# Optimization experiments

Hardware: AMD Instinct MI355X
Metric: run time of the kernel (lower is better)

Reference implementation:

```python
import jax, jax.numpy as jnp
import numpy as np

B, D_TCF, T, GAF_DIM, DK, HIDDEN, N_CLASSES = 128, 512, 1024, 256, 32, 64, 4
EPS = 1e-5

def _glorot(key, shape):
    fan_out, fan_in = shape
    lim = float(np.sqrt(6.0 / (fan_in + fan_out)))
    return jax.random.uniform(key, shape, jnp.float32, -lim, lim)

def setup_inputs() -> dict:
    key = jax.random.key(0)
    ks = jax.random.split(key, 8)
    return {
        "tcf_feat": jax.random.normal(ks[0], (B, D_TCF, T), jnp.float32),
        "gaf_emb": jax.random.normal(ks[1], (B, GAF_DIM), jnp.float32),
        "Wq": _glorot(ks[2], (DK, D_TCF)),        # q_proj.weight [out,in]
        "Wkv": _glorot(ks[3], (DK, GAF_DIM)),     # kv_proj.weight
        "Wout": _glorot(ks[4], (D_TCF, DK)),      # out_proj.weight
        "ln1_g": jnp.ones((D_TCF,), jnp.float32),
        "ln1_b": jnp.zeros((D_TCF,), jnp.float32),
        "W1": _glorot(ks[5], (HIDDEN, D_TCF)),
        "b1": jnp.zeros((HIDDEN,), jnp.float32),
        "ln2_g": jnp.ones((HIDDEN,), jnp.float32),
        "ln2_b": jnp.zeros((HIDDEN,), jnp.float32),
        "W2": _glorot(ks[6], (N_CLASSES, HIDDEN)),
        "b2": jnp.zeros((N_CLASSES,), jnp.float32),
    }

def _layernorm(x, g, b):
    mu = jnp.mean(x, axis=-1, keepdims=True)
    var = jnp.mean(jnp.square(x - mu), axis=-1, keepdims=True)
    return (x - mu) * jax.lax.rsqrt(var + EPS) * g + b

def reference(tcf_feat, gaf_emb, Wq, Wkv, Wout, ln1_g, ln1_b, W1, b1, ln2_g, ln2_b, W2, b2):
    scale = DK ** (-0.5)
    x = jnp.swapaxes(tcf_feat, 1, 2)                      # [B,T,d_tcf]
    Q = jnp.einsum('btd,kd->btk', x, Wq)                  # [B,T,dk]
    KV = gaf_emb @ Wkv.T                                  # [B,dk] (single key/value)
    scores = jnp.einsum('btk,bk->bt', Q, KV) * scale      # [B,T]
    w = jax.nn.softmax(scores, axis=1)                    # softmax over T (dim=1)
    attn_out = w[:, :, None] * KV[:, None, :]             # [B,T,dk]
    y = _layernorm(x + jnp.einsum('btk,dk->btd', attn_out, Wout), ln1_g, ln1_b)
    pooled = jnp.mean(y, axis=1)                          # [B,d_tcf]
    h = jax.nn.elu(_layernorm(pooled @ W1.T + b1, ln2_g, ln2_b))
    return h @ W2.T + b2                                  # [B,n_classes]
```

## Files before the change

kernel.cpp:

```cpp
#include <hip/hip_runtime.h>

#define BN 128
#define DTCF 512
#define TT 1024
#define GAF 256
#define DKK 32
#define HID 64
#define NCLS 4
#define LNEPS 1e-5f
#define SCALE 0.17677669529663687f

typedef float f4v __attribute__((ext_vector_type(4)));

__global__ __launch_bounds__(1024, 4) void k_fusedA(
    const float* __restrict__ tcf, const float* __restrict__ gaf,
    const float* __restrict__ Wq, const float* __restrict__ Wkv,
    const float* __restrict__ Wout, const float* __restrict__ W1,
    float* __restrict__ u, float* __restrict__ muu,
    float* __restrict__ r_o, float* __restrict__ S2, float* __restrict__ S3,
    float* __restrict__ W1t)
{
    int b = blockIdx.x, tid = threadIdx.x;

    if (b >= BN) {
        int e0 = (b - BN) * 4096 + tid * 4;
        int j  = e0 >> 9;
        int dd = e0 & 511;
        #pragma unroll
        for (int i = 0; i < 4; ++i)
            W1t[(dd + i) * HID + j] = W1[j * DTCF + dd + i];
        return;
    }

    __shared__ float gaf_s[GAF];
    __shared__ float kvp[DKK][8];
    __shared__ float kv_s[DKK];
    __shared__ float2 uq_s[DTCF];
    __shared__ float red[32];
    __shared__ float stats[2];

    int lane = tid & 63, wv = tid >> 6;

    if (tid < GAF) gaf_s[tid] = gaf[b * GAF + tid];
    __syncthreads();

    if ((tid & 31) < 8) {
        int k = tid >> 5, p8 = tid & 7;
        float a = 0.f;
        #pragma unroll
        for (int g = p8 * 32; g < p8 * 32 + 32; ++g)
            a += gaf_s[g] * Wkv[k * GAF + g];
        kvp[k][p8] = a;
    }
    __syncthreads();
    if (tid < DKK) {
        float a = 0.f;
        #pragma unroll
        for (int p = 0; p < 8; ++p) a += kvp[tid][p];
        kv_s[tid] = a;
    }
    __syncthreads();

    if (tid < DTCF) {
        int d = tid;
        float uu = 0.f;
        #pragma unroll
        for (int k = 0; k < DKK; ++k) uu += kv_s[k] * Wout[d * DKK + k];
        uq_s[d].x = uu;
        u[b * DTCF + d] = uu;
        float su = uu, suu = uu * uu;
        #pragma unroll
        for (int off = 32; off > 0; off >>= 1) {
            su  += __shfl_down(su, off);
            suu += __shfl_down(suu, off);
        }
        if (lane == 0) { red[wv] = su; red[16 + wv] = suu; }
    } else {
        int d = tid - DTCF;
        float qq = 0.f;
        #pragma unroll
        for (int k = 0; k < DKK; ++k) qq += kv_s[k] * Wq[k * DTCF + d];
        uq_s[d].y = qq;
    }
    __syncthreads();
    if (tid == 0) {
        float s = 0.f, ss = 0.f;
        #pragma unroll
        for (int i = 0; i < 8; ++i) { s += red[i]; ss += red[16 + i]; }
        float m = s * (1.f / DTCF);
        stats[0] = m;
        stats[1] = ss * (1.f / DTCF) - m * m;
        muu[b] = m;
    }
    __syncthreads();
    float mu_u = stats[0], var_u = stats[1];

    const float* col = tcf + (size_t)b * (DTCF * TT) + tid;
    float sx = 0.f, sxx = 0.f, sxu = 0.f, sxq = 0.f;
    #pragma unroll 16
    for (int d = 0; d < DTCF; ++d) {
        float v = col[d << 10];
        float2 uq = uq_s[d];
        sx  += v;
        sxx += v * v;
        sxu += v * uq.x;
        sxq += v * uq.y;
    }

    const float inv_d = 1.f / DTCF;
    float mx = sx * inv_d;
    float vx = sxx * inv_d - mx * mx;
    float cv = sxu * inv_d - mx * mu_u;
    float sc = sxq * SCALE;

    float m = sc;
    #pragma unroll
    for (int off = 32; off > 0; off >>= 1) m = fmaxf(m, __shfl_xor(m, off));
    if (lane == 0) red[wv] = m;
    __syncthreads();
    m = red[0];
    #pragma unroll
    for (int i = 1; i < 16; ++i) m = fmaxf(m, red[i]);

    float e = __expf(sc - m);
    float s = e;
    #pragma unroll
    for (int off = 32; off > 0; off >>= 1) s += __shfl_xor(s, off);
    if (lane == 0) red[16 + wv] = s;
    __syncthreads();
    s = 0.f;
    #pragma unroll
    for (int i = 0; i < 16; ++i) s += red[16 + i];
    float inv = 1.f / s;

    float w  = e * inv;
    float vr = vx + 2.f * w * cv + w * w * var_u;
    float rr = rsqrtf(vr + LNEPS);
    r_o[b * TT + tid] = rr;

    float s2p = rr * w, s3p = rr * mx;
    #pragma unroll
    for (int off = 32; off > 0; off >>= 1) {
        s2p += __shfl_xor(s2p, off);
        s3p += __shfl_xor(s3p, off);
    }
    __syncthreads();
    if (lane == 0) { red[wv] = s2p; red[16 + wv] = s3p; }
    __syncthreads();
    if (tid == 0) {
        float a2 = 0.f, a3 = 0.f;
        #pragma unroll
        for (int i = 0; i < 16; ++i) { a2 += red[i]; a3 += red[16 + i]; }
        S2[b] = a2 * (1.f / TT);
        S3[b] = a3 * (1.f / TT);
    }
}

__global__ __launch_bounds__(256) void k_passB(
    const float* __restrict__ tcf, const float* __restrict__ r,
    const float* __restrict__ u, const float* __restrict__ muu,
    const float* __restrict__ S2, const float* __restrict__ S3,
    const float* __restrict__ g1, const float* __restrict__ be1,
    float* __restrict__ pooled)
{
    int b = blockIdx.x, yb = blockIdx.y;
    int tid = threadIdx.x, wv = tid >> 6, lane = tid & 63;
    int d = (DTCF - 4) - yb * 4 + wv;

    const float* row = tcf + ((size_t)b * DTCF + d) * TT;
    const float* rb  = r + (size_t)b * TT;

    float acc = 0.f;
    #pragma unroll
    for (int i = 0; i < 4; ++i) {
        f4v    x  = __builtin_nontemporal_load((const f4v*)(row + i * 256 + lane * 4));
        float4 rv = *(const float4*)(rb + i * 256 + lane * 4);
        acc += rv.x * x.x + rv.y * x.y + rv.z * x.z + rv.w * x.w;
    }
    for (int off = 32; off > 0; off >>= 1) acc += __shfl_down(acc, off);

    if (lane == 0) {
        float pd = acc * (1.f / TT) - S3[b] + (u[b * DTCF + d] - muu[b]) * S2[b];
        pooled[b * DTCF + d] = g1[d] * pd + be1[d];
    }
}

__global__ __launch_bounds__(256) void k_head(
    const float* __restrict__ pooled, const float* __restrict__ W1t,
    const float* __restrict__ b1, const float* __restrict__ g2,
    const float* __restrict__ be2, const float* __restrict__ W2,
    const float* __restrict__ b2o, float* __restrict__ out)
{
    int b = blockIdx.x, tid = threadIdx.x;
    int j = tid & 63, wv = tid >> 6;
    __shared__ float p_s[DTCF];
    __shared__ float hred[4][HID];
    for (int i = tid; i < DTCF; i += 256) p_s[i] = pooled[b * DTCF + i];
    __syncthreads();

    float hp = 0.f;
    #pragma unroll 8
    for (int i = 0; i < 128; ++i) {
        int dd = wv * 128 + i;
        hp += p_s[dd] * W1t[dd * HID + j];
    }
    hred[wv][j] = hp;
    __syncthreads();

    if (wv == 0) {
        float h = hred[0][j] + hred[1][j] + hred[2][j] + hred[3][j] + b1[j];
        float mu = h;
        for (int off = 32; off > 0; off >>= 1) mu += __shfl_xor(mu, off);
        mu *= (1.f / HID);
        float df = h - mu;
        float vr = df * df;
        for (int off = 32; off > 0; off >>= 1) vr += __shfl_xor(vr, off);
        vr *= (1.f / HID);
        float hn = df * rsqrtf(vr + LNEPS) * g2[j] + be2[j];
        float he = hn > 0.f ? hn : expm1f(hn);

        #pragma unroll
        for (int c = 0; c < NCLS; ++c) {
            float v = he * W2[c * HID + j];
            for (int off = 32; off > 0; off >>= 1) v += __shfl_xor(v, off);
            if (j == 0) out[b * NCLS + c] = v + b2o[c];
        }
    }
}

extern "C" void kernel_launch(void* const* d_in, const int* in_sizes, int n_in,
                              void* d_out, int out_size, void* d_ws, size_t ws_size,
                              hipStream_t stream)
{
    const float* tcf  = (const float*)d_in[0];
    const float* gaf  = (const float*)d_in[1];
    const float* Wq   = (const float*)d_in[2];
    const float* Wkv  = (const float*)d_in[3];
    const float* Wout = (const float*)d_in[4];
    const float* ln1g = (const float*)d_in[5];
    const float* ln1b = (const float*)d_in[6];
    const float* W1   = (const float*)d_in[7];
    const float* b1   = (const float*)d_in[8];
    const float* ln2g = (const float*)d_in[9];
    const float* ln2b = (const float*)d_in[10];
    const float* W2   = (const float*)d_in[11];
    const float* b2   = (const float*)d_in[12];

    float* ws     = (float*)d_ws;
    float* u      = ws;
    float* muu    = u + BN * DTCF;
    float* r      = muu + BN;
    float* S2     = r + BN * TT;
    float* S3     = S2 + BN;
    float* pooled = S3 + BN;
    float* W1t    = pooled + BN * DTCF;

    k_fusedA<<<BN + 8, 1024, 0, stream>>>(tcf, gaf, Wq, Wkv, Wout, W1,
                                          u, muu, r, S2, S3, W1t);
    k_passB<<<dim3(BN, DTCF / 4), 256, 0, stream>>>(tcf, r, u, muu, S2, S3,
                                                    ln1g, ln1b, pooled);
    k_head<<<BN, 256, 0, stream>>>(pooled, W1t, b1, ln2g, ln2b, W2, b2,
                                   (float*)d_out);
}
```

Baseline: 424.4 us.

## Split pass-A statistics over two D halves and add separate softmax kernel

The column-statistics pass is split across two blocks per batch, each covering half of the feature dimension, which doubles the grid from 128 to 256 blocks of 1024 threads. Partial sums go to a workspace buffer and a new small kernel combines them, computes the u statistics, softmax, LayerNorm reciprocals and the S2/S3 reductions, and transposes W1. The aim is better CU occupancy on a 256-CU-class GPU, at the cost of an extra launch and an extra round trip of partial sums through global memory.

```diff
diff --git a/kernel.cpp b/kernel.cpp
--- a/kernel.cpp
+++ b/kernel.cpp
@@ -12,40 +12,24 @@
 
 typedef float f4v __attribute__((ext_vector_type(4)));
 
-__global__ __launch_bounds__(1024, 4) void k_fusedA(
+__global__ __launch_bounds__(1024) void k_A(
     const float* __restrict__ tcf, const float* __restrict__ gaf,
     const float* __restrict__ Wq, const float* __restrict__ Wkv,
-    const float* __restrict__ Wout, const float* __restrict__ W1,
-    float* __restrict__ u, float* __restrict__ muu,
-    float* __restrict__ r_o, float* __restrict__ S2, float* __restrict__ S3,
-    float* __restrict__ W1t)
-{
-    int b = blockIdx.x, tid = threadIdx.x;
-
-    if (b >= BN) {
-        int e0 = (b - BN) * 4096 + tid * 4;
-        int j  = e0 >> 9;
-        int dd = e0 & 511;
-        #pragma unroll
-        for (int i = 0; i < 4; ++i)
-            W1t[(dd + i) * HID + j] = W1[j * DTCF + dd + i];
-        return;
-    }
+    const float* __restrict__ Wout,
+    float* __restrict__ u, float* __restrict__ part)
+{
+    int b = blockIdx.x, h = blockIdx.y, tid = threadIdx.x;
 
     __shared__ float gaf_s[GAF];
     __shared__ float kvp[DKK][8];
     __shared__ float kv_s[DKK];
-    __shared__ float2 uq_s[DTCF];
-    __shared__ float red[32];
-    __shared__ float stats[2];
-
-    int lane = tid & 63, wv = tid >> 6;
+    __shared__ float2 uq_s[256];
 
     if (tid < GAF) gaf_s[tid] = gaf[b * GAF + tid];
     __syncthreads();
 
-    if ((tid & 31) < 8) {
-        int k = tid >> 5, p8 = tid & 7;
+    if (tid < 256) {
+        int k = tid >> 3, p8 = tid & 7;
         float a = 0.f;
         #pragma unroll
         for (int g = p8 * 32; g < p8 * 32 + 32; ++g)
@@ -61,45 +45,28 @@
     }
     __syncthreads();
 
-    if (tid < DTCF) {
-        int d = tid;
+    int d0 = h * 256;
+    if (tid < 256) {
+        int d = d0 + tid;
         float uu = 0.f;
         #pragma unroll
         for (int k = 0; k < DKK; ++k) uu += kv_s[k] * Wout[d * DKK + k];
-        uq_s[d].x = uu;
+        uq_s[tid].x = uu;
         u[b * DTCF + d] = uu;
-        float su = uu, suu = uu * uu;
-        #pragma unroll
-        for (int off = 32; off > 0; off >>= 1) {
-            su  += __shfl_down(su, off);
-            suu += __shfl_down(suu, off);
-        }
-        if (lane == 0) { red[wv] = su; red[16 + wv] = suu; }
-    } else {
-        int d = tid - DTCF;
+    } else if (tid < 512) {
+        int d = d0 + tid - 256;
         float qq = 0.f;
         #pragma unroll
         for (int k = 0; k < DKK; ++k) qq += kv_s[k] * Wq[k * DTCF + d];
-        uq_s[d].y = qq;
-    }
-    __syncthreads();
-    if (tid == 0) {
-        float s = 0.f, ss = 0.f;
-        #pragma unroll
-        for (int i = 0; i < 8; ++i) { s += red[i]; ss += red[16 + i]; }
-        float m = s * (1.f / DTCF);
-        stats[0] = m;
-        stats[1] = ss * (1.f / DTCF) - m * m;
-        muu[b] = m;
-    }
-    __syncthreads();
-    float mu_u = stats[0], var_u = stats[1];
-
-    const float* col = tcf + (size_t)b * (DTCF * TT) + tid;
+        uq_s[tid - 256].y = qq;
+    }
+    __syncthreads();
+
+    const float* col = tcf + ((size_t)b * DTCF + d0) * TT + tid;
     float sx = 0.f, sxx = 0.f, sxu = 0.f, sxq = 0.f;
     #pragma unroll 16
-    for (int d = 0; d < DTCF; ++d) {
-        float v = col[d << 10];
+    for (int d = 0; d < 256; ++d) {
+        float v = col[(size_t)d << 10];
         float2 uq = uq_s[d];
         sx  += v;
         sxx += v * v;
@@ -107,52 +74,127 @@
         sxq += v * uq.y;
     }
 
+    float* p = part + (size_t)((b * 2 + h) * 4) * TT + tid;
+    p[0]      = sx;
+    p[TT]     = sxx;
+    p[2 * TT] = sxu;
+    p[3 * TT] = sxq;
+}
+
+__global__ __launch_bounds__(256) void k_soft(
+    const float* __restrict__ part, const float* __restrict__ u,
+    const float* __restrict__ W1,
+    float* __restrict__ muu, float* __restrict__ r_o,
+    float* __restrict__ S2, float* __restrict__ S3, float* __restrict__ W1t)
+{
+    int bx = blockIdx.x, tid = threadIdx.x;
+
+    if (bx >= BN) {
+        int e0 = (bx - BN) * 4096 + tid * 16;
+        int j  = e0 >> 9;
+        int dd = e0 & 511;
+        #pragma unroll
+        for (int i = 0; i < 16; ++i)
+            W1t[(dd + i) * HID + j] = W1[j * DTCF + dd + i];
+        return;
+    }
+
+    int b = bx, lane = tid & 63, wv = tid >> 6;
+    __shared__ float red[16];
+    __shared__ float stats[2];
+
+    float su = 0.f, suu = 0.f;
+    for (int i = tid; i < DTCF; i += 256) {
+        float uu = u[b * DTCF + i];
+        su += uu; suu += uu * uu;
+    }
+    #pragma unroll
+    for (int off = 32; off > 0; off >>= 1) {
+        su  += __shfl_down(su, off);
+        suu += __shfl_down(suu, off);
+    }
+    if (lane == 0) { red[wv] = su; red[8 + wv] = suu; }
+    __syncthreads();
+    if (tid == 0) {
+        float s  = red[0] + red[1] + red[2] + red[3];
+        float ss = red[8] + red[9] + red[10] + red[11];
+        float m = s * (1.f / DTCF);
+        stats[0] = m;
+        stats[1] = ss * (1.f / DTCF) - m * m;
+        muu[b] = m;
+    }
+    __syncthreads();
+    float mu = stats[0], vu = stats[1];
+
+    int t0 = tid * 4;
+    float4 sx = {0,0,0,0}, sxx = {0,0,0,0}, sxu = {0,0,0,0}, sxq = {0,0,0,0};
+    #pragma unroll
+    for (int h = 0; h < 2; ++h) {
+        const float* p = part + (size_t)((b * 2 + h) * 4) * TT + t0;
+        float4 a  = *(const float4*)(p);
+        float4 bq = *(const float4*)(p + TT);
+        float4 c  = *(const float4*)(p + 2 * TT);
+        float4 dq = *(const float4*)(p + 3 * TT);
+        sx.x  += a.x;  sx.y  += a.y;  sx.z  += a.z;  sx.w  += a.w;
+        sxx.x += bq.x; sxx.y += bq.y; sxx.z += bq.z; sxx.w += bq.w;
+        sxu.x += c.x;  sxu.y += c.y;  sxu.z += c.z;  sxu.w += c.w;
+        sxq.x += dq.x; sxq.y += dq.y; sxq.z += dq.z; sxq.w += dq.w;
+    }
+
     const float inv_d = 1.f / DTCF;
-    float mx = sx * inv_d;
-    float vx = sxx * inv_d - mx * mx;
-    float cv = sxu * inv_d - mx * mu_u;
-    float sc = sxq * SCALE;
-
-    float m = sc;
+    float mx[4], vx[4], cv[4], sc[4];
+    float sxa[4]  = {sx.x, sx.y, sx.z, sx.w};
+    float sxxa[4] = {sxx.x, sxx.y, sxx.z, sxx.w};
+    float sxua[4] = {sxu.x, sxu.y, sxu.z, sxu.w};
+    float sxqa[4] = {sxq.x, sxq.y, sxq.z, sxq.w};
+    #pragma unroll
+    for (int i = 0; i < 4; ++i) {
+        mx[i] = sxa[i] * inv_d;
+        vx[i] = sxxa[i] * inv_d - mx[i] * mx[i];
+        cv[i] = sxua[i] * inv_d - mx[i] * mu;
+        sc[i] = sxqa[i] * SCALE;
+    }
+
+    float m = fmaxf(fmaxf(sc[0], sc[1]), fmaxf(sc[2], sc[3]));
     #pragma unroll
     for (int off = 32; off > 0; off >>= 1) m = fmaxf(m, __shfl_xor(m, off));
+    __syncthreads();
     if (lane == 0) red[wv] = m;
     __syncthreads();
-    m = red[0];
-    #pragma unroll
-    for (int i = 1; i < 16; ++i) m = fmaxf(m, red[i]);
-
-    float e = __expf(sc - m);
-    float s = e;
-    #pragma unroll
-    for (int off = 32; off > 0; off >>= 1) s += __shfl_xor(s, off);
-    if (lane == 0) red[16 + wv] = s;
-    __syncthreads();
-    s = 0.f;
-    #pragma unroll
-    for (int i = 0; i < 16; ++i) s += red[16 + i];
-    float inv = 1.f / s;
-
-    float w  = e * inv;
-    float vr = vx + 2.f * w * cv + w * w * var_u;
-    float rr = rsqrtf(vr + LNEPS);
-    r_o[b * TT + tid] = rr;
-
-    float s2p = rr * w, s3p = rr * mx;
+    m = fmaxf(fmaxf(red[0], red[1]), fmaxf(red[2], red[3]));
+
+    float e[4], sum = 0.f;
+    #pragma unroll
+    for (int i = 0; i < 4; ++i) { e[i] = __expf(sc[i] - m); sum += e[i]; }
+    #pragma unroll
+    for (int off = 32; off > 0; off >>= 1) sum += __shfl_xor(sum, off);
+    if (lane == 0) red[4 + wv] = sum;
+    __syncthreads();
+    sum = red[4] + red[5] + red[6] + red[7];
+    float inv = 1.f / sum;
+
+    float rr4[4], s2a = 0.f, s3a = 0.f;
+    #pragma unroll
+    for (int i = 0; i < 4; ++i) {
+        float w = e[i] * inv;
+        float vr = vx[i] + 2.f * w * cv[i] + w * w * vu;
+        float rr = rsqrtf(vr + LNEPS);
+        rr4[i] = rr;
+        s2a += rr * w;
+        s3a += rr * mx[i];
+    }
+    *(float4*)(r_o + (size_t)b * TT + t0) = make_float4(rr4[0], rr4[1], rr4[2], rr4[3]);
+
     #pragma unroll
     for (int off = 32; off > 0; off >>= 1) {
-        s2p += __shfl_xor(s2p, off);
-        s3p += __shfl_xor(s3p, off);
-    }
-    __syncthreads();
-    if (lane == 0) { red[wv] = s2p; red[16 + wv] = s3p; }
+        s2a += __shfl_xor(s2a, off);
+        s3a += __shfl_xor(s3a, off);
+    }
+    if (lane == 0) { red[8 + wv] = s2a; red[12 + wv] = s3a; }
     __syncthreads();
     if (tid == 0) {
-        float a2 = 0.f, a3 = 0.f;
-        #pragma unroll
-        for (int i = 0; i < 16; ++i) { a2 += red[i]; a3 += red[16 + i]; }
-        S2[b] = a2 * (1.f / TT);
-        S3[b] = a3 * (1.f / TT);
+        S2[b] = (red[8] + red[9] + red[10] + red[11]) * (1.f / TT);
+        S3[b] = (red[12] + red[13] + red[14] + red[15]) * (1.f / TT);
     }
 }
 
@@ -254,9 +296,10 @@
     float* S3     = S2 + BN;
     float* pooled = S3 + BN;
     float* W1t    = pooled + BN * DTCF;
-
-    k_fusedA<<<BN + 8, 1024, 0, stream>>>(tcf, gaf, Wq, Wkv, Wout, W1,
-                                          u, muu, r, S2, S3, W1t);
+    float* part   = W1t + DTCF * HID;
+
+    k_A<<<dim3(BN, 2), 1024, 0, stream>>>(tcf, gaf, Wq, Wkv, Wout, u, part);
+    k_soft<<<BN + 8, 256, 0, stream>>>(part, u, W1, muu, r, S2, S3, W1t);
     k_passB<<<dim3(BN, DTCF / 4), 256, 0, stream>>>(tcf, r, u, muu, S2, S3,
                                                     ln1g, ln1b, pooled);
     k_head<<<BN, 256, 0, stream>>>(pooled, W1t, b1, ln2g, ln2b, W2, b2,
```

Result: no change. 425.4 us (+0.2%).
